# Kernel optimization log

Hardware: AMD Instinct MI355X
Metric: run time of the kernel (lower is better)

## Reference

```python
import jax, jax.numpy as jnp
import numpy as np
import math

B, C_IN, C_OUT, H, W = 16, 128, 128, 56, 56
K, S, P, D = 3, 1, 1, 1
PROD_KS = K * K


def _unfold(x, k, s, p, d):
    # torch.nn.functional.unfold equivalent -> (B, k*k, C, Ho*Wo)
    b, c, h, w = x.shape
    ho = (h + 2 * p - d * (k - 1) - 1) // s + 1
    wo = (w + 2 * p - d * (k - 1) - 1) // s + 1
    xp = jnp.pad(x, ((0, 0), (0, 0), (p, p), (p, p)))
    patches = [
        xp[:, :, i * d: i * d + (ho - 1) * s + 1: s, j * d: j * d + (wo - 1) * s + 1: s]
        for i in range(k) for j in range(k)
    ]
    u = jnp.stack(patches, axis=1)  # (B, K2, C, Ho, Wo)
    return u.reshape(b, k * k, c, ho * wo), ho, wo


def setup_inputs() -> dict:
    key = jax.random.key(0)
    k1, k2, k3, k4 = jax.random.split(key, 4)
    stdv = 1.0 / math.sqrt(C_IN * PROD_KS)
    x = jax.random.normal(k1, (B, C_IN, H, W), dtype=jnp.float32)
    weight = jax.random.uniform(k2, (1, PROD_KS, C_OUT, C_IN), dtype=jnp.float32,
                                minval=-stdv, maxval=stdv)
    b_k = jax.random.uniform(k3, (1, PROD_KS, 1, C_OUT, 1), dtype=jnp.float32,
                             minval=-stdv, maxval=stdv)
    bias = jax.random.uniform(k4, (C_OUT,), dtype=jnp.float32, minval=-stdv, maxval=stdv)
    return {"x": x, "weight": weight, "b_k": b_k, "bias": bias}


def reference(x, weight, b_k, bias):
    batch = x.shape[0]
    u, ho, wo = _unfold(x, K, S, P, D)          # (B, K2, C_in, L)
    inpt = u.transpose(0, 1, 3, 2)               # (B, K2, L, C_in)
    # GEMM: (B,K2,L,Cin) x (K2,Cout,Cin) -> (B,K2,L,Cout)
    out = jnp.einsum('bklc,koc->bklo', inpt, weight[0])
    bk = b_k[0, :, 0, :, 0]                      # (K2, Cout)
    # fused cos/sin contraction over kernel positions -> (B, L, Cout) each
    a = jnp.einsum('bklo,ko->blo', out, jnp.cos(bk))
    bb = jnp.einsum('bklo,ko->blo', out, jnp.sin(bk))
    eps = 1e-05
    a_gt = a > 0
    b_gt = bb > 0
    ab_eq = a_gt == b_gt
    theta = jnp.where(ab_eq, jnp.arctan(bb / (a + eps)), -jnp.arctan(a / (bb + eps)))
    pi = math.pi
    peak = jnp.where(ab_eq & a_gt, pi / 2.0,
           jnp.where(ab_eq & ~a_gt, -pi / 2.0,
           jnp.where(~ab_eq & ~b_gt, -pi, 0.0)))
    theta = peak - theta
    o = jnp.sin(theta) * a + jnp.cos(theta) * bb  # (B, L, Cout)
    o = o.transpose(0, 2, 1) + bias[None, :, None]  # (B, Cout, L)
    conv_out = o.reshape(batch, C_OUT, ho, wo)
    theta_out = (theta / pi).transpose(0, 2, 1).reshape(batch, C_OUT, ho, wo)
    return jnp.concatenate([conv_out, theta_out], axis=1)
```

## Files before the change

kernel.cpp:

```cpp
#include <hip/hip_runtime.h>
#include <hip/hip_bf16.h>
#include <math.h>

#define NB   16
#define CIN  128
#define COUT 128
#define HH   56
#define WW   56
#define LL   3136

typedef __attribute__((ext_vector_type(8))) short short8;
typedef __attribute__((ext_vector_type(16))) float f32x16;
typedef __attribute__((ext_vector_type(4))) float f32x4;
typedef __attribute__((ext_vector_type(4))) unsigned int uint4v;

#define PXT    256
#define NPXT   13
#define XC     58
#define XPLANE 7424
#define XUSH   14848
#define XUNITS 1856
#define XHALF  928
#define CPW    16
#define WS_TAP 1024
#define WS_N   9216
#define WBYTES 36864

#define XT_ROWS 62
#define XT_PLANE_USH (XT_ROWS*XC*16)
#define XT_CG_STRIDE 3682304

#define CSD_OFF 256
#define WSP_OFF 32768
#define XT_OFF  1212416
#define XT_SIZE 29458432
#define WL_OFF  (XT_OFF + XT_SIZE)

__global__ void prep_w_kernel(const float* __restrict__ w, const float* __restrict__ bk,
                              double* __restrict__ csd, unsigned short* __restrict__ wsp) {
    int i = blockIdx.x * 256 + threadIdx.x;
    if (i >= 9*COUT*CIN) return;
    int k = i / (COUT*CIN);
    int rem = i - k*(COUT*CIN);
    int oc = rem >> 7, c = rem & 127;
    double bkv = (double)bk[k*COUT + oc];
    double ck = cos(bkv), sk = sin(bkv);
    if (c == 0) {
        csd[k*COUT + oc]          = ck;
        csd[9*COUT + k*COUT + oc] = sk;
    }
    float wv = w[i];
    float fa = (float)(ck * (double)wv);
    float fb = (float)(sk * (double)wv);
    __hip_bfloat16 ah = __float2bfloat16(fa);
    __hip_bfloat16 al = __float2bfloat16(fa - __bfloat162float(ah));
    __hip_bfloat16 bh = __float2bfloat16(fb);
    __hip_bfloat16 bl = __float2bfloat16(fb - __bfloat162float(bh));
    int ocb = oc >> 5;
    int rowa = oc & 31, rowb = 32 + rowa;
    int cg = c >> 4, cp = c & 15;
    int sl = (((cp >> 3) ^ ((rowa >> 2) & 1)) << 3) | (cp & 7);
    size_t img = ((size_t)ocb*8 + cg) * (WBYTES/2);
    wsp[img + (size_t)k*WS_TAP + rowa*CPW + sl]        = *(unsigned short*)&ah;
    wsp[img + (size_t)k*WS_TAP + rowb*CPW + sl]        = *(unsigned short*)&bh;
    wsp[img + WS_N + (size_t)k*WS_TAP + rowa*CPW + sl] = *(unsigned short*)&al;
    wsp[img + WS_N + (size_t)k*WS_TAP + rowb*CPW + sl] = *(unsigned short*)&bl;
}

__global__ void prep_x_kernel(const float* __restrict__ x, unsigned short* __restrict__ xt) {
    int i = blockIdx.x * 256 + threadIdx.x;
    if (i < 100352) {
        int c4 = i % 14; int t = i / 14;
        int row1 = t % 56; t /= 56;
        int bat = t & 15, cg = t >> 4;
        const float* xp = x + ((size_t)(bat*CIN + cg*16))*LL + row1*WW + c4*4;
        unsigned short hi[4][16], lo[4][16];
        #pragma unroll
        for (int j = 0; j < 16; j++) {
            f32x4 v = *(const f32x4*)(xp + (size_t)j*LL);
            #pragma unroll
            for (int cc = 0; cc < 4; cc++) {
                float f = v[cc];
                __hip_bfloat16 h = __float2bfloat16(f);
                __hip_bfloat16 l = __float2bfloat16(f - __bfloat162float(h));
                hi[cc][j] = *(unsigned short*)&h;
                lo[cc][j] = *(unsigned short*)&l;
            }
        }
        size_t base = ((((size_t)cg*16 + bat)*2 + 0)*XT_ROWS + (row1+1))*XC + (c4*4 + 1);
        #pragma unroll
        for (int cc = 0; cc < 4; cc++) {
            unsigned short* dh = xt + (base + cc)*16;
            unsigned short* dl = dh + XT_PLANE_USH;
            *(uint4v*)dh       = *(const uint4v*)&hi[cc][0];
            *(uint4v*)(dh + 8) = *(const uint4v*)&hi[cc][8];
            *(uint4v*)dl       = *(const uint4v*)&lo[cc][0];
            *(uint4v*)(dl + 8) = *(const uint4v*)&lo[cc][8];
        }
    } else {
        int i2 = i - 100352;
        int unit = i2 % 460; int t = i2 / 460;
        int pl = t & 1; t >>= 1;
        int bat = t & 15, cg = t >> 4;
        int row, c58;
        if (unit < 348) {
            int zr = unit / 58; c58 = unit - zr*58;
            row = (zr == 0) ? 0 : (56 + zr);
        } else {
            int u2 = unit - 348; row = 1 + (u2 >> 1); c58 = (u2 & 1) ? 57 : 0;
        }
        size_t base = ((((size_t)cg*16 + bat)*2 + pl)*XT_ROWS + row)*XC + c58;
        uint4v zz = {0u,0u,0u,0u};
        *(uint4v*)(xt + base*16)     = zz;
        *(uint4v*)(xt + base*16 + 8) = zz;
    }
}

__global__ __launch_bounds__(256, 3)
void mfma_kernel(const unsigned short* __restrict__ xt, const unsigned short* __restrict__ wsp,
                 const float* __restrict__ bias, float* __restrict__ out,
                 unsigned* __restrict__ cnt, unsigned* __restrict__ wl, unsigned cap)
{
    __shared__ __align__(16) unsigned short SM[XUSH];
    __shared__ float sm_bias[32];

    const int tid = threadIdx.x;
    int bid = blockIdx.x;
    int wk = (bid & 7) * (NB*NPXT*4/8) + (bid >> 3);
    const int ocb = wk & 3; wk >>= 2;
    const int pxt = wk % NPXT;
    const int bat = wk / NPXT;
    const int l0  = pxt * PXT;
    const int o0  = ocb * 32;
    const int yf  = l0 / WW;

    const int lane = tid & 63;
    const int n    = lane & 31;
    const int kh   = lane >> 5;
    const int wave = tid >> 6;

    if (tid < 32) sm_bias[tid] = bias[o0 + tid];

    unsigned xoff[8];
    #pragma unroll
    for (int k = 0; k < 8; k++) {
        int u = tid + 256*k;
        int uc = u < XUNITS ? u : XUNITS-1;
        int pl = uc >= XHALF ? 1 : 0;
        int rem = uc - pl*XHALF;
        int q  = rem >> 1;
        int hl = rem & 1;
        int hg = hl ^ ((q >> 2) & 1);
        int r  = q / XC;
        int c  = q - r*XC;
        xoff[k] = (unsigned)((((bat*2 + pl)*XT_ROWS + (yf + r))*XC + c)*32 + hg*16);
    }

    int q0g[2];
    #pragma unroll
    for (int g = 0; g < 2; g++) {
        int p  = l0 + wave*64 + g*32 + n;
        int pc = p < LL ? p : LL-1;
        int py = pc / WW, pxx = pc - py*WW;
        q0g[g] = (py - yf)*XC + pxx;
    }
    const int sw  = ((((n>>2)&1) ^ kh) << 3);
    const int iAa = n*CPW + sw;
    const int iAb = (32+n)*CPW + sw;

    f32x16 acc_a[2], acc_b[2];
    #pragma unroll
    for (int g = 0; g < 2; g++) {
        #pragma unroll
        for (int r = 0; r < 16; r++) { acc_a[g][r] = 0.f; acc_b[g][r] = 0.f; }
    }

    const char* xtB  = (const char*)xt;
    const char* wspB = (const char*)wsp + (size_t)ocb * (8*(size_t)WBYTES);

    auto stage = [&](int chn) {
        const char* xp = xtB + (size_t)chn * XT_CG_STRIDE;
        #pragma unroll
        for (int k = 0; k < 7; k++) {
            __builtin_amdgcn_global_load_lds(
                (const __attribute__((address_space(1))) unsigned int*)(xp + xoff[k]),
                (__attribute__((address_space(3))) unsigned int*)&SM[(wave*64 + 256*k)*8],
                16, 0, 0);
        }
        if (wave == 0)
            __builtin_amdgcn_global_load_lds(
                (const __attribute__((address_space(1))) unsigned int*)(xp + xoff[7]),
                (__attribute__((address_space(3))) unsigned int*)&SM[1792*8],
                16, 0, 0);
    };

    short8 wbuf[2][4];
    auto ldw = [&](int chn, int tap, short8* dst) {
        const char* tp = wspB + (size_t)chn*WBYTES + tap*(WS_TAP*2);
        dst[0] = *(const short8*)(tp + iAa*2);
        dst[1] = *(const short8*)(tp + iAb*2);
        dst[2] = *(const short8*)(tp + 2*WS_N + iAa*2);
        dst[3] = *(const short8*)(tp + 2*WS_N + iAb*2);
    };

    stage(0);
    ldw(0, 0, wbuf[0]);
    ldw(0, 1, wbuf[1]);
    __syncthreads();

    #pragma unroll 1
    for (int ch = 0; ch < 8; ch++) {
        #pragma unroll
        for (int tap = 0; tap < 9; tap++) {
            const int ky = tap / 3, kx = tap - 3*ky;
            short8 Aha = wbuf[tap&1][0];
            short8 Ahb = wbuf[tap&1][1];
            short8 Ala = wbuf[tap&1][2];
            short8 Alb = wbuf[tap&1][3];
            if (tap < 7) ldw(ch, tap+2, wbuf[tap&1]);
            __builtin_amdgcn_s_setprio(1);
            #pragma unroll
            for (int g = 0; g < 2; g++) {
                int q  = q0g[g] + ky*XC + kx;
                int si = q*16 + ((kh ^ ((q>>2)&1)) << 3);
                short8 Bh = *(const short8*)&SM[si];
                short8 Bl = *(const short8*)&SM[XPLANE + si];
                acc_a[g] = __builtin_amdgcn_mfma_f32_32x32x16_bf16(Ala, Bh, acc_a[g], 0,0,0);
                acc_a[g] = __builtin_amdgcn_mfma_f32_32x32x16_bf16(Aha, Bl, acc_a[g], 0,0,0);
                acc_a[g] = __builtin_amdgcn_mfma_f32_32x32x16_bf16(Aha, Bh, acc_a[g], 0,0,0);
                acc_b[g] = __builtin_amdgcn_mfma_f32_32x32x16_bf16(Alb, Bh, acc_b[g], 0,0,0);
                acc_b[g] = __builtin_amdgcn_mfma_f32_32x32x16_bf16(Ahb, Bl, acc_b[g], 0,0,0);
                acc_b[g] = __builtin_amdgcn_mfma_f32_32x32x16_bf16(Ahb, Bh, acc_b[g], 0,0,0);
            }
            __builtin_amdgcn_s_setprio(0);
        }
        if (ch < 7) {
            ldw(ch+1, 0, wbuf[0]);
            ldw(ch+1, 1, wbuf[1]);
            __syncthreads();
            stage(ch+1);
            __syncthreads();
        }
    }

    const float eps = 1e-05f;
    const float PIf = 3.14159265358979323846f;
    size_t obase = (size_t)bat * (2*COUT) * LL;

    #pragma unroll
    for (int g = 0; g < 2; g++) {
        const int pcol = wave*64 + g*32 + n;
        const int p = l0 + pcol;
        #pragma unroll
        for (int r = 0; r < 16; r++) {
            int row = (r & 3) + 8*(r >> 2) + 4*kh;
            float av = acc_a[g][r];
            float bv = acc_b[g][r];
            bool flag = (p < LL) &&
                        (fabsf(av) < 1.5e-4f || (bv < 1.05e-5f && bv > -2.05e-5f));
            unsigned long long m = __ballot(flag);
            if (m) {
                int leader = (int)__ffsll((long long)m) - 1;
                unsigned base = 0;
                if (lane == leader) base = atomicAdd(cnt, (unsigned)__popcll(m));
                base = __shfl(base, leader);
                if (flag) {
                    unsigned slot = base + (unsigned)__popcll(m & ((1ULL << lane) - 1ULL));
                    if (slot < cap)
                        wl[slot] = ((unsigned)(bat*LL + p) << 7) | (unsigned)(o0 + row);
                }
            }
            bool ag = av > 0.f, bg = bv > 0.f;
            bool eq = (ag == bg);
            float ratio = eq ? (bv / (av + eps)) : (av / (bv + eps));
            float at = atanf(ratio);
            if (!eq) at = -at;
            float peak = eq ? (ag ? PIf*0.5f : -PIf*0.5f) : (bg ? 0.0f : -PIf);
            float th = peak - at;
            if (p < LL) {
                out[obase + (size_t)(o0+row)*LL + p]      = sinf(th)*av + cosf(th)*bv + sm_bias[row];
                out[obase + (size_t)(COUT+o0+row)*LL + p] = th * (1.0f/PIf);
            }
        }
    }
}

__global__ __launch_bounds__(256)
void fixup_kernel(const float* __restrict__ x, const float* __restrict__ w,
                  const double* __restrict__ csd, const float* __restrict__ bias,
                  const unsigned* __restrict__ cnt, const unsigned* __restrict__ wl,
                  unsigned cap, float* __restrict__ out) {
    const int lane   = threadIdx.x & 63;
    const int waveid = (blockIdx.x * 256 + threadIdx.x) >> 6;
    const int nwaves = gridDim.x * 4;
    unsigned nf = *cnt; if (nf > cap) nf = cap;
    const double PI = 3.14159265358979323846;

    for (unsigned u = waveid; u < nf; u += nwaves) {
        unsigned idx = wl[u];
        int oc = idx & 127;
        unsigned rest = idx >> 7;
        int bb_ = rest / LL;
        int l   = rest - bb_*LL;
        int yy  = l / WW;
        int xx  = l - yy*WW;
        const float* xb = x + (size_t)bb_ * CIN * LL;

        double pa = 0.0, pb = 0.0;
        #pragma unroll
        for (int k = 0; k < 9; k++) {
            int dy = k/3, dx = k - dy*3;
            int py = yy + dy - 1, px = xx + dx - 1;
            double pk = 0.0;
            if ((unsigned)py < HH && (unsigned)px < WW) {
                int base = py*WW + px;
                const float* wr = w + k*(COUT*CIN) + oc*CIN;
                int c = lane;
                pk  = (double)xb[(size_t)c*LL + base] * (double)wr[c];
                c = lane + 64;
                pk += (double)xb[(size_t)c*LL + base] * (double)wr[c];
            }
            pa += csd[k*COUT + oc] * pk;
            pb += csd[9*COUT + k*COUT + oc] * pk;
        }
        #pragma unroll
        for (int off = 32; off > 0; off >>= 1) {
            pa += __shfl_xor(pa, off, 64);
            pb += __shfl_xor(pb, off, 64);
        }
        if (lane == 0) {
            bool ag = pa > 0.0, bg = pb > 0.0;
            bool eq = (ag == bg);
            double th;
            if (eq) th = (ag ? PI*0.5 : -PI*0.5) - atan(pb / (pa + 1e-5));
            else    th = (bg ? 0.0 : -PI) + atan(pa / (pb + 1e-5));
            double o = sin(th)*pa + cos(th)*pb + (double)bias[oc];
            out[((size_t)bb_*(2*COUT) + oc) * LL + l]        = (float)o;
            out[((size_t)bb_*(2*COUT) + COUT + oc) * LL + l] = (float)(th / PI);
        }
    }
}

extern "C" void kernel_launch(void* const* d_in, const int* in_sizes, int n_in,
                              void* d_out, int out_size, void* d_ws, size_t ws_size,
                              hipStream_t stream) {
    const float* x    = (const float*)d_in[0];
    const float* w    = (const float*)d_in[1];
    const float* bk   = (const float*)d_in[2];
    const float* bias = (const float*)d_in[3];
    float* out = (float*)d_out;

    char* ws = (char*)d_ws;
    unsigned*       cnt = (unsigned*)ws;
    double*         csd = (double*)(ws + CSD_OFF);
    unsigned short* wsp = (unsigned short*)(ws + WSP_OFF);
    unsigned short* xt  = (unsigned short*)(ws + XT_OFF);
    unsigned*       wl  = (unsigned*)(ws + WL_OFF);
    unsigned cap = (ws_size > (size_t)WL_OFF + 4096) ? (unsigned)((ws_size - WL_OFF) / 4) : 0u;

    hipMemsetAsync(cnt, 0, 4, stream);
    hipLaunchKernelGGL(prep_w_kernel,   dim3(576),  dim3(256), 0, stream, w, bk, csd, wsp);
    hipLaunchKernelGGL(prep_x_kernel,   dim3(852),  dim3(256), 0, stream, x, xt);
    hipLaunchKernelGGL(mfma_kernel,     dim3(NB*NPXT*4), dim3(256), 0, stream,
                       xt, wsp, bias, out, cnt, wl, cap);
    hipLaunchKernelGGL(fixup_kernel,    dim3(512),  dim3(256), 0, stream,
                       x, w, csd, bias, cnt, wl, cap, out);
}
```

Before: 335.2 us.

## Merge prep kernels, double-buffer LDS staging with 8 waves, simplify epilogue trig

The weight and input prep kernels are merged into a single launch that also zeroes the worklist counter, which removes the memset and one kernel launch. The MFMA kernel now runs 512 threads per block, with each wave owning one 32-pixel group. LDS is double-buffered so the next channel group's input is staged while the current one is computed, which drops one barrier per iteration. The epilogue replaces sinf/cosf of theta with an algebraic form built from 1/sqrt(1+ratio^2), and the fixup grid is halved; this raises LDS use per block and may change occupancy and rounding.

```diff
diff --git a/kernel.cpp b/kernel.cpp
--- a/kernel.cpp
+++ b/kernel.cpp
@@ -36,97 +36,101 @@
 #define XT_SIZE 29458432
 #define WL_OFF  (XT_OFF + XT_SIZE)
 
-__global__ void prep_w_kernel(const float* __restrict__ w, const float* __restrict__ bk,
-                              double* __restrict__ csd, unsigned short* __restrict__ wsp) {
-    int i = blockIdx.x * 256 + threadIdx.x;
-    if (i >= 9*COUT*CIN) return;
-    int k = i / (COUT*CIN);
-    int rem = i - k*(COUT*CIN);
-    int oc = rem >> 7, c = rem & 127;
-    double bkv = (double)bk[k*COUT + oc];
-    double ck = cos(bkv), sk = sin(bkv);
-    if (c == 0) {
-        csd[k*COUT + oc]          = ck;
-        csd[9*COUT + k*COUT + oc] = sk;
-    }
-    float wv = w[i];
-    float fa = (float)(ck * (double)wv);
-    float fb = (float)(sk * (double)wv);
-    __hip_bfloat16 ah = __float2bfloat16(fa);
-    __hip_bfloat16 al = __float2bfloat16(fa - __bfloat162float(ah));
-    __hip_bfloat16 bh = __float2bfloat16(fb);
-    __hip_bfloat16 bl = __float2bfloat16(fb - __bfloat162float(bh));
-    int ocb = oc >> 5;
-    int rowa = oc & 31, rowb = 32 + rowa;
-    int cg = c >> 4, cp = c & 15;
-    int sl = (((cp >> 3) ^ ((rowa >> 2) & 1)) << 3) | (cp & 7);
-    size_t img = ((size_t)ocb*8 + cg) * (WBYTES/2);
-    wsp[img + (size_t)k*WS_TAP + rowa*CPW + sl]        = *(unsigned short*)&ah;
-    wsp[img + (size_t)k*WS_TAP + rowb*CPW + sl]        = *(unsigned short*)&bh;
-    wsp[img + WS_N + (size_t)k*WS_TAP + rowa*CPW + sl] = *(unsigned short*)&al;
-    wsp[img + WS_N + (size_t)k*WS_TAP + rowb*CPW + sl] = *(unsigned short*)&bl;
-}
-
-__global__ void prep_x_kernel(const float* __restrict__ x, unsigned short* __restrict__ xt) {
-    int i = blockIdx.x * 256 + threadIdx.x;
-    if (i < 100352) {
-        int c4 = i % 14; int t = i / 14;
-        int row1 = t % 56; t /= 56;
-        int bat = t & 15, cg = t >> 4;
-        const float* xp = x + ((size_t)(bat*CIN + cg*16))*LL + row1*WW + c4*4;
-        unsigned short hi[4][16], lo[4][16];
-        #pragma unroll
-        for (int j = 0; j < 16; j++) {
-            f32x4 v = *(const f32x4*)(xp + (size_t)j*LL);
+__global__ void prep_kernel(const float* __restrict__ w, const float* __restrict__ bk,
+                            const float* __restrict__ x,
+                            double* __restrict__ csd, unsigned short* __restrict__ wsp,
+                            unsigned short* __restrict__ xt, unsigned* __restrict__ cnt) {
+    int bid = blockIdx.x;
+    if (bid == 0 && threadIdx.x == 0) *cnt = 0u;
+    if (bid < 576) {
+        int i = bid * 256 + threadIdx.x;
+        if (i >= 9*COUT*CIN) return;
+        int k = i / (COUT*CIN);
+        int rem = i - k*(COUT*CIN);
+        int oc = rem >> 7, c = rem & 127;
+        double bkv = (double)bk[k*COUT + oc];
+        double ck = cos(bkv), sk = sin(bkv);
+        if (c == 0) {
+            csd[k*COUT + oc]          = ck;
+            csd[9*COUT + k*COUT + oc] = sk;
+        }
+        float wv = w[i];
+        float fa = (float)(ck * (double)wv);
+        float fb = (float)(sk * (double)wv);
+        __hip_bfloat16 ah = __float2bfloat16(fa);
+        __hip_bfloat16 al = __float2bfloat16(fa - __bfloat162float(ah));
+        __hip_bfloat16 bh = __float2bfloat16(fb);
+        __hip_bfloat16 bl = __float2bfloat16(fb - __bfloat162float(bh));
+        int ocb = oc >> 5;
+        int rowa = oc & 31, rowb = 32 + rowa;
+        int cg = c >> 4, cp = c & 15;
+        int sl = (((cp >> 3) ^ ((rowa >> 2) & 1)) << 3) | (cp & 7);
+        size_t img = ((size_t)ocb*8 + cg) * (WBYTES/2);
+        wsp[img + (size_t)k*WS_TAP + rowa*CPW + sl]        = *(unsigned short*)&ah;
+        wsp[img + (size_t)k*WS_TAP + rowb*CPW + sl]        = *(unsigned short*)&bh;
+        wsp[img + WS_N + (size_t)k*WS_TAP + rowa*CPW + sl] = *(unsigned short*)&al;
+        wsp[img + WS_N + (size_t)k*WS_TAP + rowb*CPW + sl] = *(unsigned short*)&bl;
+    } else {
+        int i = (bid - 576) * 256 + threadIdx.x;
+        if (i < 100352) {
+            int c4 = i % 14; int t = i / 14;
+            int row1 = t % 56; t /= 56;
+            int bat = t & 15, cg = t >> 4;
+            const float* xp = x + ((size_t)(bat*CIN + cg*16))*LL + row1*WW + c4*4;
+            unsigned short hi[4][16], lo[4][16];
+            #pragma unroll
+            for (int j = 0; j < 16; j++) {
+                f32x4 v = *(const f32x4*)(xp + (size_t)j*LL);
+                #pragma unroll
+                for (int cc = 0; cc < 4; cc++) {
+                    float f = v[cc];
+                    __hip_bfloat16 h = __float2bfloat16(f);
+                    __hip_bfloat16 l = __float2bfloat16(f - __bfloat162float(h));
+                    hi[cc][j] = *(unsigned short*)&h;
+                    lo[cc][j] = *(unsigned short*)&l;
+                }
+            }
+            size_t base = ((((size_t)cg*16 + bat)*2 + 0)*XT_ROWS + (row1+1))*XC + (c4*4 + 1);
             #pragma unroll
             for (int cc = 0; cc < 4; cc++) {
-                float f = v[cc];
-                __hip_bfloat16 h = __float2bfloat16(f);
-                __hip_bfloat16 l = __float2bfloat16(f - __bfloat162float(h));
-                hi[cc][j] = *(unsigned short*)&h;
-                lo[cc][j] = *(unsigned short*)&l;
-            }
-        }
-        size_t base = ((((size_t)cg*16 + bat)*2 + 0)*XT_ROWS + (row1+1))*XC + (c4*4 + 1);
-        #pragma unroll
-        for (int cc = 0; cc < 4; cc++) {
-            unsigned short* dh = xt + (base + cc)*16;
-            unsigned short* dl = dh + XT_PLANE_USH;
-            *(uint4v*)dh       = *(const uint4v*)&hi[cc][0];
-            *(uint4v*)(dh + 8) = *(const uint4v*)&hi[cc][8];
-            *(uint4v*)dl       = *(const uint4v*)&lo[cc][0];
-            *(uint4v*)(dl + 8) = *(const uint4v*)&lo[cc][8];
-        }
-    } else {
-        int i2 = i - 100352;
-        int unit = i2 % 460; int t = i2 / 460;
-        int pl = t & 1; t >>= 1;
-        int bat = t & 15, cg = t >> 4;
-        int row, c58;
-        if (unit < 348) {
-            int zr = unit / 58; c58 = unit - zr*58;
-            row = (zr == 0) ? 0 : (56 + zr);
-        } else {
-            int u2 = unit - 348; row = 1 + (u2 >> 1); c58 = (u2 & 1) ? 57 : 0;
-        }
-        size_t base = ((((size_t)cg*16 + bat)*2 + pl)*XT_ROWS + row)*XC + c58;
-        uint4v zz = {0u,0u,0u,0u};
-        *(uint4v*)(xt + base*16)     = zz;
-        *(uint4v*)(xt + base*16 + 8) = zz;
+                unsigned short* dh = xt + (base + cc)*16;
+                unsigned short* dl = dh + XT_PLANE_USH;
+                *(uint4v*)dh       = *(const uint4v*)&hi[cc][0];
+                *(uint4v*)(dh + 8) = *(const uint4v*)&hi[cc][8];
+                *(uint4v*)dl       = *(const uint4v*)&lo[cc][0];
+                *(uint4v*)(dl + 8) = *(const uint4v*)&lo[cc][8];
+            }
+        } else if (i < 218112) {
+            int i2 = i - 100352;
+            int unit = i2 % 460; int t = i2 / 460;
+            int pl = t & 1; t >>= 1;
+            int bat = t & 15, cg = t >> 4;
+            int row, c58;
+            if (unit < 348) {
+                int zr = unit / 58; c58 = unit - zr*58;
+                row = (zr == 0) ? 0 : (56 + zr);
+            } else {
+                int u2 = unit - 348; row = 1 + (u2 >> 1); c58 = (u2 & 1) ? 57 : 0;
+            }
+            size_t base = ((((size_t)cg*16 + bat)*2 + pl)*XT_ROWS + row)*XC + c58;
+            uint4v zz = {0u,0u,0u,0u};
+            *(uint4v*)(xt + base*16)     = zz;
+            *(uint4v*)(xt + base*16 + 8) = zz;
+        }
     }
 }
 
-__global__ __launch_bounds__(256, 3)
+__global__ __launch_bounds__(512, 4)
 void mfma_kernel(const unsigned short* __restrict__ xt, const unsigned short* __restrict__ wsp,
                  const float* __restrict__ bias, float* __restrict__ out,
                  unsigned* __restrict__ cnt, unsigned* __restrict__ wl, unsigned cap)
 {
-    __shared__ __align__(16) unsigned short SM[XUSH];
+    __shared__ __align__(16) unsigned short SM[2*XUSH];
     __shared__ float sm_bias[32];
 
     const int tid = threadIdx.x;
     int bid = blockIdx.x;
-    int wk = (bid & 7) * (NB*NPXT*4/8) + (bid >> 3);
+    int wk = (bid & 7) * 104 + (bid >> 3);
     const int ocb = wk & 3; wk >>= 2;
     const int pxt = wk % NPXT;
     const int bat = wk / NPXT;
@@ -141,10 +145,10 @@
 
     if (tid < 32) sm_bias[tid] = bias[o0 + tid];
 
-    unsigned xoff[8];
+    unsigned xoff[4];
     #pragma unroll
-    for (int k = 0; k < 8; k++) {
-        int u = tid + 256*k;
+    for (int k = 0; k < 4; k++) {
+        int u = tid + 512*k;
         int uc = u < XUNITS ? u : XUNITS-1;
         int pl = uc >= XHALF ? 1 : 0;
         int rem = uc - pl*XHALF;
@@ -156,41 +160,36 @@
         xoff[k] = (unsigned)((((bat*2 + pl)*XT_ROWS + (yf + r))*XC + c)*32 + hg*16);
     }
 
-    int q0g[2];
-    #pragma unroll
-    for (int g = 0; g < 2; g++) {
-        int p  = l0 + wave*64 + g*32 + n;
-        int pc = p < LL ? p : LL-1;
-        int py = pc / WW, pxx = pc - py*WW;
-        q0g[g] = (py - yf)*XC + pxx;
-    }
+    int p  = l0 + wave*32 + n;
+    int pc = p < LL ? p : LL-1;
+    int py = pc / WW, pxx = pc - py*WW;
+    const int q0 = (py - yf)*XC + pxx;
+
     const int sw  = ((((n>>2)&1) ^ kh) << 3);
     const int iAa = n*CPW + sw;
     const int iAb = (32+n)*CPW + sw;
 
-    f32x16 acc_a[2], acc_b[2];
+    f32x16 acc_a, acc_b;
     #pragma unroll
-    for (int g = 0; g < 2; g++) {
-        #pragma unroll
-        for (int r = 0; r < 16; r++) { acc_a[g][r] = 0.f; acc_b[g][r] = 0.f; }
-    }
+    for (int r = 0; r < 16; r++) { acc_a[r] = 0.f; acc_b[r] = 0.f; }
 
     const char* xtB  = (const char*)xt;
     const char* wspB = (const char*)wsp + (size_t)ocb * (8*(size_t)WBYTES);
 
-    auto stage = [&](int chn) {
+    auto stage = [&](int bsel, int chn) {
         const char* xp = xtB + (size_t)chn * XT_CG_STRIDE;
+        unsigned short* smb = &SM[bsel*XUSH];
         #pragma unroll
-        for (int k = 0; k < 7; k++) {
+        for (int k = 0; k < 3; k++) {
             __builtin_amdgcn_global_load_lds(
                 (const __attribute__((address_space(1))) unsigned int*)(xp + xoff[k]),
-                (__attribute__((address_space(3))) unsigned int*)&SM[(wave*64 + 256*k)*8],
+                (__attribute__((address_space(3))) unsigned int*)&smb[(wave*64 + 512*k)*8],
                 16, 0, 0);
         }
-        if (wave == 0)
+        if (wave < 5)
             __builtin_amdgcn_global_load_lds(
-                (const __attribute__((address_space(1))) unsigned int*)(xp + xoff[7]),
-                (__attribute__((address_space(3))) unsigned int*)&SM[1792*8],
+                (const __attribute__((address_space(1))) unsigned int*)(xp + xoff[3]),
+                (__attribute__((address_space(3))) unsigned int*)&smb[(1536 + wave*64)*8],
                 16, 0, 0);
     };
 
@@ -203,13 +202,15 @@
         dst[3] = *(const short8*)(tp + 2*WS_N + iAb*2);
     };
 
-    stage(0);
+    stage(0, 0);
     ldw(0, 0, wbuf[0]);
     ldw(0, 1, wbuf[1]);
     __syncthreads();
 
     #pragma unroll 1
     for (int ch = 0; ch < 8; ch++) {
+        if (ch < 7) stage((ch+1)&1, ch+1);
+        const unsigned short* smb = &SM[(ch&1)*XUSH];
         #pragma unroll
         for (int tap = 0; tap < 9; tap++) {
             const int ky = tap / 3, kx = tap - 3*ky;
@@ -218,69 +219,64 @@
             short8 Ala = wbuf[tap&1][2];
             short8 Alb = wbuf[tap&1][3];
             if (tap < 7) ldw(ch, tap+2, wbuf[tap&1]);
+            int q  = q0 + ky*XC + kx;
+            int si = q*16 + ((kh ^ ((q>>2)&1)) << 3);
+            short8 Bh = *(const short8*)&smb[si];
+            short8 Bl = *(const short8*)&smb[XPLANE + si];
             __builtin_amdgcn_s_setprio(1);
-            #pragma unroll
-            for (int g = 0; g < 2; g++) {
-                int q  = q0g[g] + ky*XC + kx;
-                int si = q*16 + ((kh ^ ((q>>2)&1)) << 3);
-                short8 Bh = *(const short8*)&SM[si];
-                short8 Bl = *(const short8*)&SM[XPLANE + si];
-                acc_a[g] = __builtin_amdgcn_mfma_f32_32x32x16_bf16(Ala, Bh, acc_a[g], 0,0,0);
-                acc_a[g] = __builtin_amdgcn_mfma_f32_32x32x16_bf16(Aha, Bl, acc_a[g], 0,0,0);
-                acc_a[g] = __builtin_amdgcn_mfma_f32_32x32x16_bf16(Aha, Bh, acc_a[g], 0,0,0);
-                acc_b[g] = __builtin_amdgcn_mfma_f32_32x32x16_bf16(Alb, Bh, acc_b[g], 0,0,0);
-                acc_b[g] = __builtin_amdgcn_mfma_f32_32x32x16_bf16(Ahb, Bl, acc_b[g], 0,0,0);
-                acc_b[g] = __builtin_amdgcn_mfma_f32_32x32x16_bf16(Ahb, Bh, acc_b[g], 0,0,0);
-            }
+            acc_a = __builtin_amdgcn_mfma_f32_32x32x16_bf16(Ala, Bh, acc_a, 0,0,0);
+            acc_a = __builtin_amdgcn_mfma_f32_32x32x16_bf16(Aha, Bl, acc_a, 0,0,0);
+            acc_a = __builtin_amdgcn_mfma_f32_32x32x16_bf16(Aha, Bh, acc_a, 0,0,0);
+            acc_b = __builtin_amdgcn_mfma_f32_32x32x16_bf16(Alb, Bh, acc_b, 0,0,0);
+            acc_b = __builtin_amdgcn_mfma_f32_32x32x16_bf16(Ahb, Bl, acc_b, 0,0,0);
+            acc_b = __builtin_amdgcn_mfma_f32_32x32x16_bf16(Ahb, Bh, acc_b, 0,0,0);
             __builtin_amdgcn_s_setprio(0);
         }
         if (ch < 7) {
             ldw(ch+1, 0, wbuf[0]);
             ldw(ch+1, 1, wbuf[1]);
             __syncthreads();
-            stage(ch+1);
-            __syncthreads();
         }
     }
 
     const float eps = 1e-05f;
     const float PIf = 3.14159265358979323846f;
     size_t obase = (size_t)bat * (2*COUT) * LL;
+    const int pcol = wave*32 + n;
+    const int pp = l0 + pcol;
 
     #pragma unroll
-    for (int g = 0; g < 2; g++) {
-        const int pcol = wave*64 + g*32 + n;
-        const int p = l0 + pcol;
-        #pragma unroll
-        for (int r = 0; r < 16; r++) {
-            int row = (r & 3) + 8*(r >> 2) + 4*kh;
-            float av = acc_a[g][r];
-            float bv = acc_b[g][r];
-            bool flag = (p < LL) &&
-                        (fabsf(av) < 1.5e-4f || (bv < 1.05e-5f && bv > -2.05e-5f));
-            unsigned long long m = __ballot(flag);
-            if (m) {
-                int leader = (int)__ffsll((long long)m) - 1;
-                unsigned base = 0;
-                if (lane == leader) base = atomicAdd(cnt, (unsigned)__popcll(m));
-                base = __shfl(base, leader);
-                if (flag) {
-                    unsigned slot = base + (unsigned)__popcll(m & ((1ULL << lane) - 1ULL));
-                    if (slot < cap)
-                        wl[slot] = ((unsigned)(bat*LL + p) << 7) | (unsigned)(o0 + row);
-                }
-            }
-            bool ag = av > 0.f, bg = bv > 0.f;
-            bool eq = (ag == bg);
-            float ratio = eq ? (bv / (av + eps)) : (av / (bv + eps));
-            float at = atanf(ratio);
-            if (!eq) at = -at;
-            float peak = eq ? (ag ? PIf*0.5f : -PIf*0.5f) : (bg ? 0.0f : -PIf);
-            float th = peak - at;
-            if (p < LL) {
-                out[obase + (size_t)(o0+row)*LL + p]      = sinf(th)*av + cosf(th)*bv + sm_bias[row];
-                out[obase + (size_t)(COUT+o0+row)*LL + p] = th * (1.0f/PIf);
-            }
+    for (int r = 0; r < 16; r++) {
+        int row = (r & 3) + 8*(r >> 2) + 4*kh;
+        float av = acc_a[r];
+        float bv = acc_b[r];
+        bool flag = (pp < LL) &&
+                    (fabsf(av) < 1.5e-4f || (bv < 1.05e-5f && bv > -2.05e-5f));
+        unsigned long long m = __ballot(flag);
+        if (m) {
+            int leader = (int)__ffsll((long long)m) - 1;
+            unsigned base = 0;
+            if (lane == leader) base = atomicAdd(cnt, (unsigned)__popcll(m));
+            base = __shfl(base, leader);
+            if (flag) {
+                unsigned slot = base + (unsigned)__popcll(m & ((1ULL << lane) - 1ULL));
+                if (slot < cap)
+                    wl[slot] = ((unsigned)(bat*LL + pp) << 7) | (unsigned)(o0 + row);
+            }
+        }
+        bool ag = av > 0.f, bg = bv > 0.f;
+        bool eq = (ag == bg);
+        float ratio = eq ? (bv / (av + eps)) : (av / (bv + eps));
+        float at = atanf(ratio);
+        float peak = eq ? (ag ? PIf*0.5f : -PIf*0.5f) : (bg ? 0.0f : -PIf);
+        float th = peak - (eq ? at : -at);
+        float c = 1.0f / sqrtf(1.0f + ratio*ratio);
+        float t = eq ? (av + ratio*bv) : (ratio*av + bv);
+        bool pos = eq ? ag : bg;
+        float o = (pos ? c : -c) * t;
+        if (pp < LL) {
+            out[obase + (size_t)(o0+row)*LL + pp]      = o + sm_bias[row];
+            out[obase + (size_t)(COUT+o0+row)*LL + pp] = th * (1.0f/PIf);
         }
     }
 }
@@ -358,11 +354,10 @@
     unsigned*       wl  = (unsigned*)(ws + WL_OFF);
     unsigned cap = (ws_size > (size_t)WL_OFF + 4096) ? (unsigned)((ws_size - WL_OFF) / 4) : 0u;
 
-    hipMemsetAsync(cnt, 0, 4, stream);
-    hipLaunchKernelGGL(prep_w_kernel,   dim3(576),  dim3(256), 0, stream, w, bk, csd, wsp);
-    hipLaunchKernelGGL(prep_x_kernel,   dim3(852),  dim3(256), 0, stream, x, xt);
-    hipLaunchKernelGGL(mfma_kernel,     dim3(NB*NPXT*4), dim3(256), 0, stream,
+    hipLaunchKernelGGL(prep_kernel,  dim3(1428), dim3(256), 0, stream,
+                       w, bk, x, csd, wsp, xt, cnt);
+    hipLaunchKernelGGL(mfma_kernel,  dim3(NB*NPXT*4), dim3(512), 0, stream,
                        xt, wsp, bias, out, cnt, wl, cap);
-    hipLaunchKernelGGL(fixup_kernel,    dim3(512),  dim3(256), 0, stream,
+    hipLaunchKernelGGL(fixup_kernel, dim3(256), dim3(256), 0, stream,
                        x, w, csd, bias, cnt, wl, cap, out);
 }
```

Result: slower. 356.6 us (+6.4%).
